# Performance work log

Hardware: AMD Instinct MI355X
Metric: run time of the kernel (lower is better)

## Reference

```python
import jax, jax.numpy as jnp
import numpy as np

B, SQ, SK, H, NH = 2, 2048, 2048, 2048, 16
HD = H // NH  # 128
NEG = -1e9


def setup_inputs() -> dict:
    key = jax.random.key(0)
    ks = jax.random.split(key, 8)
    hidden_states = jax.random.normal(ks[0], (B, SQ, H), dtype=jnp.float32)
    # key already transposed/expanded for baddbmm: [B*nh, head_dim, key_len]
    k = jax.random.normal(ks[1], (B * NH, HD, SK), dtype=jnp.float32)
    v = jax.random.normal(ks[2], (B, NH, SK, HD), dtype=jnp.float32)
    # additive float causal mask [B, 1, Sq, Sk]
    causal = jnp.tril(jnp.ones((SQ, SK), dtype=bool))
    attention_mask = jnp.where(causal, 0.0, NEG).astype(jnp.float32)
    attention_mask = jnp.broadcast_to(attention_mask[None, None], (B, 1, SQ, SK))
    w_q = jax.random.normal(ks[3], (H, H), dtype=jnp.float32) * 0.02
    b_q = jnp.zeros((H,), dtype=jnp.float32)
    w_proj = jax.random.normal(ks[4], (H, H), dtype=jnp.float32) * 0.02
    b_proj = jnp.zeros((H,), dtype=jnp.float32)
    return {
        "hidden_states": hidden_states,
        "key": k,
        "value": v,
        "attention_mask": attention_mask,
        "w_q": w_q,
        "b_q": b_q,
        "w_proj": w_proj,
        "b_proj": b_proj,
    }


def reference(hidden_states, key, value, attention_mask, w_q, b_q, w_proj, b_proj):
    dtype = hidden_states.dtype
    scale = 1.0 / (HD ** 0.5)  # scale_attn_weights=True, attention_multiplier=None
    # q projection: [B, Sq, H] -> [B, nh, Sq, hd]
    q = hidden_states @ w_q.T + b_q
    q = q.reshape(B, SQ, NH, HD).transpose(0, 2, 1, 3)
    # key comes in as [B*nh, hd, Sk]
    k = key.reshape(B, NH, HD, SK)
    # scores = mask + scale * q @ k  (baddbmm with beta=1)
    scores = attention_mask + scale * jnp.einsum("bhqd,bhdk->bhqk", q, k)
    # softmax in fp32 (attention_softmax_in_fp32=True), cast back
    probs = jax.nn.softmax(scores.astype(jnp.float32), axis=-1).astype(dtype)
    # attn_pdrop=0 -> no dropout
    out = jnp.einsum("bhqk,bhkd->bhqd", probs, value)  # [B, nh, Sq, hd]
    out = out.transpose(0, 2, 1, 3).reshape(B, SQ, H)
    out = out @ w_proj.T + b_proj  # resid_pdrop=0 -> no dropout
    return out
```

## Files before the change

### kernel.cpp

```cpp
#include <hip/hip_runtime.h>
#include <hip/hip_bf16.h>

typedef __bf16 bf16;
typedef __bf16 bf16x4 __attribute__((ext_vector_type(4)));
typedef __bf16 bf16x8 __attribute__((ext_vector_type(8)));
typedef float  f32x4  __attribute__((ext_vector_type(4)));
typedef float  f32x16 __attribute__((ext_vector_type(16)));
typedef unsigned int u32;

#define B_   2
#define SQ_  2048
#define SK_  2048
#define H_   2048
#define NH_  16
#define HD_  128
#define BH_  (B_*NH_)

__device__ inline void gl_lds16(const bf16* g, bf16* l) {
  __builtin_amdgcn_global_load_lds(
      (const __attribute__((address_space(1))) u32*)(const void*)g,
      (__attribute__((address_space(3))) u32*)(void*)l,
      16, 0, 0);
}

__device__ inline float exp2_fast(float x) {
  float r; asm("v_exp_f32 %0, %1" : "=v"(r) : "v"(x)); return r;
}

union PW { u32 w[4]; bf16x8 v; };

__global__ __launch_bounds__(256) void cvt3_f32_bf16(const float* __restrict__ a, bf16* __restrict__ ao,
                                                     const float* __restrict__ b, bf16* __restrict__ bo,
                                                     const float* __restrict__ c, bf16* __restrict__ co) {
  const int blk = blockIdx.x;
  const float* in; bf16* out; int n4, bstart, nblk;
  if (blk < 1024)      { in = a; out = ao; n4 = (B_ * SQ_ * H_) / 4; bstart = 0;    nblk = 1024; }
  else if (blk < 1536) { in = b; out = bo; n4 = (H_ * H_) / 4;       bstart = 1024; nblk = 512; }
  else                 { in = c; out = co; n4 = (H_ * H_) / 4;       bstart = 1536; nblk = 512; }
  int i = (blk - bstart) * 256 + threadIdx.x;
  const int stride = nblk * 256;
  for (; i < n4; i += stride) {
    float4 v = ((const float4*)in)[i];
    bf16x4 w; w[0] = (bf16)v.x; w[1] = (bf16)v.y; w[2] = (bf16)v.z; w[3] = (bf16)v.w;
    ((bf16x4*)out)[i] = w;
  }
}

__global__ __launch_bounds__(256) void transpose_cvt2(const float* __restrict__ key,
                                                      const float* __restrict__ value,
                                                      bf16* __restrict__ kout,
                                                      bf16* __restrict__ vout) {
  __shared__ float tile[64][65];
  const int id = blockIdx.x;
  const float* src; bf16* dst; int R, C, r0, c0, bh;
  if (id < 2048) {
    src = key; dst = kout; R = HD_; C = SK_;
    c0 = (id & 31) * 64; r0 = ((id >> 5) & 1) * 64; bh = id >> 6;
  } else {
    const int j = id - 2048;
    src = value; dst = vout; R = SK_; C = HD_;
    c0 = (j & 1) * 64; r0 = ((j >> 1) & 31) * 64; bh = j >> 6;
  }
  src += (size_t)bh * R * C;
  dst += (size_t)bh * R * C;
  const int t = threadIdx.x;
  const int tx = t & 15, ty = t >> 4;
#pragma unroll
  for (int p = 0; p < 4; ++p) {
    int rr = ty + p * 16;
    float4 v = *(const float4*)&src[(size_t)(r0 + rr) * C + c0 + tx * 4];
    tile[rr][tx * 4 + 0] = v.x; tile[rr][tx * 4 + 1] = v.y;
    tile[rr][tx * 4 + 2] = v.z; tile[rr][tx * 4 + 3] = v.w;
  }
  __syncthreads();
#pragma unroll
  for (int p = 0; p < 4; ++p) {
    int cc = ty + p * 16;
    bf16x4 w;
#pragma unroll
    for (int i = 0; i < 4; ++i) w[i] = (bf16)tile[tx * 4 + i][cc];
    *(bf16x4*)&dst[(size_t)(c0 + cc) * R + r0 + tx * 4] = w;
  }
}

template <typename OutT>
__global__ __launch_bounds__(256) void gemm_bt(const bf16* __restrict__ A,
                                               const bf16* __restrict__ Bw,
                                               const float* __restrict__ bias,
                                               OutT* __restrict__ C,
                                               int M, int N, int K, float osc) {
  __shared__ bf16 Abuf[128 * 32];
  __shared__ bf16 Bbuf[128 * 32];
  const int nbn = N >> 7;
  int wg = blockIdx.x, nwg = gridDim.x;
  int swz = (nwg & 7) ? wg : ((wg & 7) * (nwg >> 3) + (wg >> 3));
  int bm = swz / nbn, bn = swz % nbn;
  const int t = threadIdx.x, lane = t & 63, wid = t >> 6;
  const int r = lane & 15, g = lane >> 4;
  const int wr = wid >> 1, wc = wid & 1;
  const size_t m0 = (size_t)bm * 128, n0 = (size_t)bn * 128;

  f32x4 acc[4][4];
#pragma unroll
  for (int m = 0; m < 4; ++m)
#pragma unroll
    for (int n = 0; n < 4; ++n) acc[m][n] = (f32x4){0.f, 0.f, 0.f, 0.f};

  for (int k0 = 0; k0 < K; k0 += 32) {
    __syncthreads();
#pragma unroll
    for (int p = 0; p < 2; ++p) {
      int c = p * 256 + t;
      int row = c >> 2, off = c & 3;
      gl_lds16(A + (m0 + row) * K + k0 + off * 8, &Abuf[(p * 256 + wid * 64) * 8]);
      gl_lds16(Bw + (n0 + row) * K + k0 + off * 8, &Bbuf[(p * 256 + wid * 64) * 8]);
    }
    __syncthreads();
    bf16x8 af[4], bfr[4];
#pragma unroll
    for (int m = 0; m < 4; ++m)
      af[m] = *(const bf16x8*)&Abuf[(wr * 64 + m * 16 + r) * 32 + g * 8];
#pragma unroll
    for (int n = 0; n < 4; ++n)
      bfr[n] = *(const bf16x8*)&Bbuf[(wc * 64 + n * 16 + r) * 32 + g * 8];
#pragma unroll
    for (int m = 0; m < 4; ++m)
#pragma unroll
      for (int n = 0; n < 4; ++n)
        acc[m][n] = __builtin_amdgcn_mfma_f32_16x16x32_bf16(af[m], bfr[n], acc[m][n], 0, 0, 0);
  }

  float bv[4];
#pragma unroll
  for (int n = 0; n < 4; ++n) bv[n] = bias[n0 + wc * 64 + n * 16 + r];
#pragma unroll
  for (int m = 0; m < 4; ++m)
#pragma unroll
    for (int n = 0; n < 4; ++n)
#pragma unroll
      for (int rr = 0; rr < 4; ++rr) {
        size_t row = m0 + wr * 64 + m * 16 + g * 4 + rr;
        size_t col = n0 + wc * 64 + n * 16 + r;
        C[row * N + col] = (OutT)((acc[m][n][rr] + bv[n]) * osc);
      }
}

__global__ __launch_bounds__(256, 2) void flash_attn(const bf16* __restrict__ Q,
                                                     const bf16* __restrict__ Kt,
                                                     const bf16* __restrict__ Vt,
                                                     bf16* __restrict__ O,
                                                     bf16* __restrict__ part,
                                                     float2* __restrict__ mlbuf) {
  __shared__ bf16 Klds[2][64 * 128];
  __shared__ bf16 Vlds[2][128 * 64];

  const int id = blockIdx.x;
  const int pr = (id >> 3) & 7;
  const int hf = (id >> 6) & 1;
  const int bh = (id & 7) + 8 * (id >> 7);
  const int qtA = 15 - pr, qtB = pr;
  const int nA = 2 * qtA + 2, nB = 2 * qtB + 2;
  const int b = bh >> 4, h = bh & 15;
  const int t = threadIdx.x, lane = t & 63, wid = t >> 6;
  const int l5 = lane & 31, hiL = lane >> 5;

  const bf16* Kbase = Kt + (size_t)bh * SK_ * HD_;
  const bf16* Vbase = Vt + (size_t)bh * HD_ * SK_;

  u32 kSrc[4], vSrc[4];
#pragma unroll
  for (int p = 0; p < 4; ++p) {
    int c = p * 256 + t;
    { int row = c >> 4, off = c & 15, src = off ^ (row & 7);
      kSrc[p] = (u32)(row * HD_ + src * 8); }
    { int row = c >> 3, off = c & 7, src = off ^ (row & 7);
      vSrc[p] = (u32)(row * SK_ + src * 8); }
  }

  int cur = 0;
  const int npass = hf ? 2 : 1;
#pragma unroll 1
  for (int ps = 0; ps < npass; ++ps) {
    int qt, lo, hi, partial;
    if (!hf)          { qt = qtA; lo = 0;  hi = 17; partial = 1; }
    else if (ps == 0) { qt = qtA; lo = 17; hi = nA; partial = 1; }
    else              { qt = qtB; lo = 0;  hi = nB; partial = 0; }
    const int qbw = qt * 128 + wid * 32;
    const int q_lane = qbw + l5;

    bf16x8 qf[8];
    {
      const size_t qrow = (size_t)(b * SQ_ + q_lane) * H_ + (size_t)h * HD_;
#pragma unroll
      for (int dt = 0; dt < 8; ++dt)
        qf[dt] = *(const bf16x8*)&Q[qrow + dt * 16 + 8 * hiL];
    }

    f32x16 acc[4];
#pragma unroll
    for (int n = 0; n < 4; ++n)
#pragma unroll
      for (int e = 0; e < 16; ++e) acc[n][e] = 0.f;
    float mrun = -3.0e38f, lpart = 0.f;

    {
      const size_t ks = (size_t)lo * (64 * HD_), vs = (size_t)lo * 64;
#pragma unroll
      for (int p = 0; p < 4; ++p) {
        gl_lds16(Kbase + ks + kSrc[p], &Klds[cur][(p * 256 + wid * 64) * 8]);
        gl_lds16(Vbase + vs + vSrc[p], &Vlds[cur][(p * 256 + wid * 64) * 8]);
      }
    }
    asm volatile("s_waitcnt vmcnt(0)" ::: "memory");
    __syncthreads();

#pragma unroll 1
    for (int st = lo; st < hi; ++st) {
      if (st + 1 < hi) {
        const size_t ks = (size_t)(st + 1) * (64 * HD_), vs = (size_t)(st + 1) * 64;
#pragma unroll
        for (int p = 0; p < 4; ++p) {
          gl_lds16(Kbase + ks + kSrc[p], &Klds[cur ^ 1][(p * 256 + wid * 64) * 8]);
          gl_lds16(Vbase + vs + vSrc[p], &Vlds[cur ^ 1][(p * 256 + wid * 64) * 8]);
        }
      }
      const int s0 = st * 64;

      if (s0 <= qbw + 31) {
        f32x16 sv0, sv1;
#pragma unroll
        for (int e = 0; e < 16; ++e) { sv0[e] = 0.f; sv1[e] = 0.f; }
        __builtin_amdgcn_s_setprio(1);
#pragma unroll
        for (int dt = 0; dt < 8; ++dt) {
          const int dch = ((2 * dt + hiL) ^ (l5 & 7)) * 8;
          bf16x8 kf0 = *(const bf16x8*)&Klds[cur][l5 * 128 + dch];
          bf16x8 kf1 = *(const bf16x8*)&Klds[cur][(32 + l5) * 128 + dch];
          sv0 = __builtin_amdgcn_mfma_f32_32x32x16_bf16(kf0, qf[dt], sv0, 0, 0, 0);
          sv1 = __builtin_amdgcn_mfma_f32_32x32x16_bf16(kf1, qf[dt], sv1, 0, 0, 0);
        }
        __builtin_amdgcn_s_setprio(0);

        if (s0 + 63 > qbw) {
#pragma unroll
          for (int r2 = 0; r2 < 16; ++r2) {
            const int kl = (r2 & 3) + 8 * (r2 >> 2) + 4 * hiL;
            if (s0 + kl > q_lane)      sv0[r2] = -3.0e38f;
            if (s0 + 32 + kl > q_lane) sv1[r2] = -3.0e38f;
          }
        }

        float pm = -3.0e38f;
#pragma unroll
        for (int r2 = 0; r2 < 16; ++r2) pm = fmaxf(pm, fmaxf(sv0[r2], sv1[r2]));
        pm = fmaxf(pm, __shfl_xor(pm, 32));
        if (!__all(pm <= mrun + 10.0f ? 1 : 0)) {
          const float mnew = fmaxf(mrun, pm);
          const float corr = exp2_fast(mrun - mnew);
          mrun = mnew;
          lpart *= corr;
          const int cb = __float_as_int(corr);
#pragma unroll
          for (int r2 = 0; r2 < 16; ++r2) {
            const int q2 = (r2 & 3) + 8 * (r2 >> 2) + 4 * hiL;
            const float cc = __int_as_float(__builtin_amdgcn_ds_bpermute(q2 * 4, cb));
#pragma unroll
            for (int n = 0; n < 4; ++n) acc[n][r2] *= cc;
          }
        }

        float psum = 0.f;
#pragma unroll
        for (int r2 = 0; r2 < 16; ++r2) {
          sv0[r2] = exp2_fast(sv0[r2] - mrun); psum += sv0[r2];
          sv1[r2] = exp2_fast(sv1[r2] - mrun); psum += sv1[r2];
        }
        lpart += psum;

        bf16x8 pa[4];
#pragma unroll
        for (int h2 = 0; h2 < 2; ++h2) {
          u32 pk[8], px[8];
#pragma unroll
          for (int j = 0; j < 8; ++j) {
            union { bf16 hh[2]; u32 u; } tt;
            float plo = h2 ? sv1[2 * j] : sv0[2 * j];
            float phi = h2 ? sv1[2 * j + 1] : sv0[2 * j + 1];
            tt.hh[0] = (bf16)plo; tt.hh[1] = (bf16)phi;
            pk[j] = tt.u;
          }
#pragma unroll
          for (int j = 0; j < 8; ++j) px[j] = (u32)__shfl_xor((int)pk[j], 32);
          PW a0, a1;
          a0.w[0] = hiL ? px[2] : pk[0];
          a0.w[1] = hiL ? px[3] : pk[1];
          a0.w[2] = hiL ? pk[2] : px[0];
          a0.w[3] = hiL ? pk[3] : px[1];
          a1.w[0] = hiL ? px[6] : pk[4];
          a1.w[1] = hiL ? px[7] : pk[5];
          a1.w[2] = hiL ? pk[6] : px[4];
          a1.w[3] = hiL ? pk[7] : px[5];
          pa[2 * h2]     = a0.v;
          pa[2 * h2 + 1] = a1.v;
        }

        __builtin_amdgcn_s_setprio(1);
#pragma unroll
        for (int n = 0; n < 4; ++n) {
#pragma unroll
          for (int kt = 0; kt < 4; ++kt) {
            bf16x8 vf = *(const bf16x8*)&Vlds[cur][(n * 32 + l5) * 64 +
                                                   (((2 * kt + hiL) ^ (l5 & 7)) * 8)];
            acc[n] = __builtin_amdgcn_mfma_f32_32x32x16_bf16(pa[kt], vf, acc[n], 0, 0, 0);
          }
        }
        __builtin_amdgcn_s_setprio(0);
      }

      asm volatile("s_waitcnt vmcnt(0)" ::: "memory");
      __syncthreads();
      cur ^= 1;
    }

    float ltot = lpart + __shfl_xor(lpart, 32);
    if (partial) {
      const int slot = (hf * 8 + pr) * 32 + bh;
      bf16* pbase = part + (size_t)slot * (128 * 128);
#pragma unroll
      for (int n = 0; n < 4; ++n)
#pragma unroll
        for (int r2 = 0; r2 < 16; ++r2) {
          const int rowt = wid * 32 + (r2 & 3) + 8 * (r2 >> 2) + 4 * hiL;
          pbase[rowt * 128 + n * 32 + l5] = (bf16)acc[n][r2];
        }
      if (lane < 32)
        mlbuf[(size_t)slot * 128 + wid * 32 + lane] = float2{mrun, ltot};
    } else {
      const float inv = 1.0f / ltot;
      const int ib = __float_as_int(inv);
#pragma unroll
      for (int r2 = 0; r2 < 16; ++r2) {
        const int q2 = (r2 & 3) + 8 * (r2 >> 2) + 4 * hiL;
        const float ic = __int_as_float(__builtin_amdgcn_ds_bpermute(q2 * 4, ib));
        const size_t rowg = (size_t)(b * SQ_ + qbw + q2);
#pragma unroll
        for (int n = 0; n < 4; ++n)
          O[rowg * H_ + (size_t)h * HD_ + n * 32 + l5] = (bf16)(acc[n][r2] * ic);
      }
    }
  }
}

__global__ __launch_bounds__(256) void flash_merge(const bf16* __restrict__ part,
                                                   const float2* __restrict__ mlbuf,
                                                   bf16* __restrict__ O) {
  const int idx = blockIdx.x * 2 + (threadIdx.x >> 7);
  const int d = threadIdx.x & 127;
  const int row = idx & 127;
  const int bh = (idx >> 7) & 31;
  const int pr = idx >> 12;
  const int qtA = 15 - pr;
  const int b = bh >> 4, h = bh & 15;
  const int slot0 = pr * 32 + bh;
  const int slot1 = (8 + pr) * 32 + bh;
  const float2 ml0 = mlbuf[(size_t)slot0 * 128 + row];
  const float2 ml1 = mlbuf[(size_t)slot1 * 128 + row];
  const float M = fmaxf(ml0.x, ml1.x);
  const float c0 = exp2_fast(ml0.x - M);
  const float c1 = exp2_fast(ml1.x - M);
  const float inv = 1.0f / (c0 * ml0.y + c1 * ml1.y);
  const float a0 = (float)part[(size_t)slot0 * (128 * 128) + row * 128 + d];
  const float a1 = (float)part[(size_t)slot1 * (128 * 128) + row * 128 + d];
  const size_t orow = (size_t)(b * SQ_ + qtA * 128 + row);
  O[orow * H_ + (size_t)h * HD_ + d] = (bf16)((c0 * a0 + c1 * a1) * inv);
}

extern "C" void kernel_launch(void* const* d_in, const int* in_sizes, int n_in,
                              void* d_out, int out_size, void* d_ws, size_t ws_size,
                              hipStream_t stream) {
  const float* hidden = (const float*)d_in[0];
  const float* key    = (const float*)d_in[1];
  const float* value  = (const float*)d_in[2];
  const float* w_q    = (const float*)d_in[4];
  const float* b_q    = (const float*)d_in[5];
  const float* w_proj = (const float*)d_in[6];
  const float* b_proj = (const float*)d_in[7];
  float* out = (float*)d_out;

  const size_t N_HID = (size_t)B_ * SQ_ * H_;
  const size_t N_W   = (size_t)H_ * H_;
  const size_t N_KV  = (size_t)BH_ * SK_ * HD_;
  const float SC2 = 0.08838834764831845f * 1.4426950408889634f;

  bf16* hid_bf  = (bf16*)d_ws;
  bf16* wq_bf   = hid_bf + N_HID;
  bf16* wp_bf   = wq_bf + N_W;
  bf16* k_bf    = wp_bf + N_W;
  bf16* vt_bf   = k_bf + N_KV;
  bf16* q_bf    = vt_bf + N_KV;
  bf16* part_bf = q_bf + N_HID;
  float2* ml_bf = (float2*)(part_bf + (size_t)512 * 128 * 128);
  bf16* attn_bf = hid_bf;

  cvt3_f32_bf16<<<2048, 256, 0, stream>>>(hidden, hid_bf, w_q, wq_bf, w_proj, wp_bf);
  transpose_cvt2<<<4096, 256, 0, stream>>>(key, value, k_bf, vt_bf);

  gemm_bt<bf16><<<(B_ * SQ_ / 128) * (H_ / 128), 256, 0, stream>>>(
      hid_bf, wq_bf, b_q, q_bf, B_ * SQ_, H_, H_, SC2);

  flash_attn<<<512, 256, 0, stream>>>(q_bf, k_bf, vt_bf, attn_bf, part_bf, ml_bf);
  flash_merge<<<16384, 256, 0, stream>>>(part_bf, ml_bf, attn_bf);

  gemm_bt<float><<<(B_ * SQ_ / 128) * (H_ / 128), 256, 0, stream>>>(
      attn_bf, wp_bf, b_proj, out, B_ * SQ_, H_, H_, 1.0f);
}
```

Baseline: 215.6 us.

## Add flash attention variant with 256-row Q tiles, 32-key steps, and 4-way KV split

Adds a new flash attention kernel in which each wave handles 64 query rows (two 32-row MFMA tiles) and shares every K/V fragment read from LDS between both tiles. The key/value step drops to 32 columns. Causal work is balanced by pairing query tiles and splitting the KV range into four equal 18-step chunks, followed by a new merge kernel that combines up to four partial results. The aim is to halve LDS K/V traffic per MFMA and even out per-block load. In exchange it adds more partial-buffer writes, a larger merge launch, and a workspace-size check that falls back to the old path.

```diff
diff --git a/kernel.cpp b/kernel.cpp
--- a/kernel.cpp
+++ b/kernel.cpp
@@ -145,6 +145,278 @@
       }
 }
 
+__device__ __forceinline__ void sm32(f32x16& sv, float& mrun, float& lpart,
+                                     f32x16 (&acc)[4], bf16x8 (&pa)[2], int hiL) {
+  float pm = sv[0];
+#pragma unroll
+  for (int r2 = 1; r2 < 16; ++r2) pm = fmaxf(pm, sv[r2]);
+  pm = fmaxf(pm, __shfl_xor(pm, 32));
+  if (!__all(pm <= mrun + 10.0f ? 1 : 0)) {
+    const float mnew = fmaxf(mrun, pm);
+    const float corr = exp2_fast(mrun - mnew);
+    mrun = mnew; lpart *= corr;
+    const int cb = __float_as_int(corr);
+#pragma unroll
+    for (int r2 = 0; r2 < 16; ++r2) {
+      const int q2 = (r2 & 3) + 8 * (r2 >> 2) + 4 * hiL;
+      const float cc = __int_as_float(__builtin_amdgcn_ds_bpermute(q2 * 4, cb));
+#pragma unroll
+      for (int n = 0; n < 4; ++n) acc[n][r2] *= cc;
+    }
+  }
+  float psum = 0.f;
+#pragma unroll
+  for (int r2 = 0; r2 < 16; ++r2) { sv[r2] = exp2_fast(sv[r2] - mrun); psum += sv[r2]; }
+  lpart += psum;
+  u32 pk[8], px[8];
+#pragma unroll
+  for (int j = 0; j < 8; ++j) {
+    union { bf16 hh[2]; u32 u; } tt;
+    tt.hh[0] = (bf16)sv[2 * j]; tt.hh[1] = (bf16)sv[2 * j + 1];
+    pk[j] = tt.u;
+  }
+#pragma unroll
+  for (int j = 0; j < 8; ++j) px[j] = (u32)__shfl_xor((int)pk[j], 32);
+  PW a0, a1;
+  a0.w[0] = hiL ? px[2] : pk[0];  a0.w[1] = hiL ? px[3] : pk[1];
+  a0.w[2] = hiL ? pk[2] : px[0];  a0.w[3] = hiL ? pk[3] : px[1];
+  a1.w[0] = hiL ? px[6] : pk[4];  a1.w[1] = hiL ? px[7] : pk[5];
+  a1.w[2] = hiL ? pk[6] : px[4];  a1.w[3] = hiL ? pk[7] : px[5];
+  pa[0] = a0.v; pa[1] = a1.v;
+}
+
+__global__ __launch_bounds__(256, 2) void flash_attn2(const bf16* __restrict__ Q,
+                                                      const bf16* __restrict__ Kt,
+                                                      const bf16* __restrict__ Vt,
+                                                      bf16* __restrict__ O,
+                                                      bf16* __restrict__ part,
+                                                      float2* __restrict__ mlbuf) {
+  __shared__ bf16 Klds[2][32 * 128];
+  __shared__ bf16 Vlds[2][128 * 32];
+
+  const int id = blockIdx.x;
+  const int pr = (id >> 3) & 3;
+  const int qq = (id >> 5) & 3;
+  const int bh = (id & 7) + 8 * (id >> 7);
+  const int qtA = 7 - pr, qtB = pr;
+  const int nA = 8 * qtA + 8, nB = 8 * qtB + 8;
+  const int prefix = pr * 4 + (pr == 3 ? 1 : 0);
+  const int b = bh >> 4, h = bh & 15;
+  const int t = threadIdx.x, lane = t & 63, wid = t >> 6;
+  const int l5 = lane & 31, hiL = lane >> 5;
+
+  const bf16* Kbase = Kt + (size_t)bh * SK_ * HD_;
+  const bf16* Vbase = Vt + (size_t)bh * HD_ * SK_;
+
+  u32 kSrc[2], vSrc[2];
+#pragma unroll
+  for (int p2 = 0; p2 < 2; ++p2) {
+    int c = p2 * 256 + t;
+    { int row = c >> 4, off = c & 15, src = off ^ (row & 7);
+      kSrc[p2] = (u32)(row * HD_ + src * 8); }
+    { int row = c >> 2, off = c & 3, src = off ^ ((row >> 1) & 3);
+      vSrc[p2] = (u32)(row * SK_ + src * 8); }
+  }
+
+  const int lo_q = qq * 18, hi_q = lo_q + 18;
+  const bool hasA = (lo_q < nA);
+  const int aHi = hi_q < nA ? hi_q : nA;
+  const int bLo = (lo_q - nA > 0) ? (lo_q - nA) : 0;
+  const int bHi = hi_q - nA;
+  const bool hasB = (hi_q > nA);
+  const int npass = (hasA ? 1 : 0) + (hasB ? 1 : 0);
+
+  int cur = 0;
+#pragma unroll 1
+  for (int p = 0; p < npass; ++p) {
+    const bool isA = hasA && (p == 0);
+    const int qt = isA ? qtA : qtB;
+    const int lo = isA ? lo_q : bLo;
+    const int hi = isA ? aHi : bHi;
+    const bool direct = (!isA) && (bLo == 0) && (bHi == nB);
+    const int slotg = (prefix + (isA ? qq : qq + 1)) * 32 + bh;
+    const int qbw = qt * 256 + wid * 64;
+
+    bf16x8 qf0[8], qf1[8];
+    {
+      const size_t qr0 = (size_t)(b * SQ_ + qbw + l5) * H_ + (size_t)h * HD_;
+      const size_t qr1 = qr0 + (size_t)32 * H_;
+#pragma unroll
+      for (int dt = 0; dt < 8; ++dt) {
+        qf0[dt] = *(const bf16x8*)&Q[qr0 + dt * 16 + 8 * hiL];
+        qf1[dt] = *(const bf16x8*)&Q[qr1 + dt * 16 + 8 * hiL];
+      }
+    }
+
+    f32x16 acc0[4], acc1[4];
+#pragma unroll
+    for (int n = 0; n < 4; ++n)
+#pragma unroll
+      for (int e = 0; e < 16; ++e) { acc0[n][e] = 0.f; acc1[n][e] = 0.f; }
+    float mrun0 = -3.0e38f, lpart0 = 0.f, mrun1 = -3.0e38f, lpart1 = 0.f;
+
+    {
+      const size_t ks = (size_t)lo * (32 * HD_), vs = (size_t)lo * 32;
+#pragma unroll
+      for (int p2 = 0; p2 < 2; ++p2) {
+        gl_lds16(Kbase + ks + kSrc[p2], &Klds[cur][(p2 * 256 + wid * 64) * 8]);
+        gl_lds16(Vbase + vs + vSrc[p2], &Vlds[cur][(p2 * 256 + wid * 64) * 8]);
+      }
+    }
+    asm volatile("s_waitcnt vmcnt(0)" ::: "memory");
+    __syncthreads();
+
+#pragma unroll 1
+    for (int st = lo; st < hi; ++st) {
+      if (st + 1 < hi) {
+        const size_t ks = (size_t)(st + 1) * (32 * HD_), vs = (size_t)(st + 1) * 32;
+#pragma unroll
+        for (int p2 = 0; p2 < 2; ++p2) {
+          gl_lds16(Kbase + ks + kSrc[p2], &Klds[cur ^ 1][(p2 * 256 + wid * 64) * 8]);
+          gl_lds16(Vbase + vs + vSrc[p2], &Vlds[cur ^ 1][(p2 * 256 + wid * 64) * 8]);
+        }
+      }
+      const int s0 = st * 32;
+      if (s0 <= qbw + 63) {
+        const bool g0a = (s0 <= qbw + 31);
+        f32x16 sv0, sv1;
+#pragma unroll
+        for (int e = 0; e < 16; ++e) { sv0[e] = 0.f; sv1[e] = 0.f; }
+        __builtin_amdgcn_s_setprio(1);
+        if (g0a) {
+#pragma unroll
+          for (int dt = 0; dt < 8; ++dt) {
+            bf16x8 kf = *(const bf16x8*)&Klds[cur][l5 * 128 + (((2 * dt + hiL) ^ (l5 & 7)) * 8)];
+            sv0 = __builtin_amdgcn_mfma_f32_32x32x16_bf16(kf, qf0[dt], sv0, 0, 0, 0);
+            sv1 = __builtin_amdgcn_mfma_f32_32x32x16_bf16(kf, qf1[dt], sv1, 0, 0, 0);
+          }
+        } else {
+#pragma unroll
+          for (int dt = 0; dt < 8; ++dt) {
+            bf16x8 kf = *(const bf16x8*)&Klds[cur][l5 * 128 + (((2 * dt + hiL) ^ (l5 & 7)) * 8)];
+            sv1 = __builtin_amdgcn_mfma_f32_32x32x16_bf16(kf, qf1[dt], sv1, 0, 0, 0);
+          }
+        }
+        __builtin_amdgcn_s_setprio(0);
+
+        if (g0a && s0 + 31 > qbw) {
+#pragma unroll
+          for (int r2 = 0; r2 < 16; ++r2) {
+            const int kl = (r2 & 3) + 8 * (r2 >> 2) + 4 * hiL;
+            if (s0 + kl > qbw + l5) sv0[r2] = -3.0e38f;
+          }
+        }
+        if (s0 + 31 > qbw + 32) {
+#pragma unroll
+          for (int r2 = 0; r2 < 16; ++r2) {
+            const int kl = (r2 & 3) + 8 * (r2 >> 2) + 4 * hiL;
+            if (s0 + kl > qbw + 32 + l5) sv1[r2] = -3.0e38f;
+          }
+        }
+
+        bf16x8 pa0[2], pa1[2];
+        if (g0a) sm32(sv0, mrun0, lpart0, acc0, pa0, hiL);
+        sm32(sv1, mrun1, lpart1, acc1, pa1, hiL);
+
+        __builtin_amdgcn_s_setprio(1);
+        if (g0a) {
+#pragma unroll
+          for (int n = 0; n < 4; ++n)
+#pragma unroll
+            for (int kt = 0; kt < 2; ++kt) {
+              bf16x8 vf = *(const bf16x8*)&Vlds[cur][(n * 32 + l5) * 32 +
+                                                     (((2 * kt + hiL) ^ ((l5 >> 1) & 3)) * 8)];
+              acc0[n] = __builtin_amdgcn_mfma_f32_32x32x16_bf16(pa0[kt], vf, acc0[n], 0, 0, 0);
+              acc1[n] = __builtin_amdgcn_mfma_f32_32x32x16_bf16(pa1[kt], vf, acc1[n], 0, 0, 0);
+            }
+        } else {
+#pragma unroll
+          for (int n = 0; n < 4; ++n)
+#pragma unroll
+            for (int kt = 0; kt < 2; ++kt) {
+              bf16x8 vf = *(const bf16x8*)&Vlds[cur][(n * 32 + l5) * 32 +
+                                                     (((2 * kt + hiL) ^ ((l5 >> 1) & 3)) * 8)];
+              acc1[n] = __builtin_amdgcn_mfma_f32_32x32x16_bf16(pa1[kt], vf, acc1[n], 0, 0, 0);
+            }
+        }
+        __builtin_amdgcn_s_setprio(0);
+      }
+      asm volatile("s_waitcnt vmcnt(0)" ::: "memory");
+      __syncthreads();
+      cur ^= 1;
+    }
+
+    const float lt0 = lpart0 + __shfl_xor(lpart0, 32);
+    const float lt1 = lpart1 + __shfl_xor(lpart1, 32);
+    if (direct) {
+      const int ib0 = __float_as_int(1.0f / lt0);
+      const int ib1 = __float_as_int(1.0f / lt1);
+#pragma unroll
+      for (int r2 = 0; r2 < 16; ++r2) {
+        const int q2 = (r2 & 3) + 8 * (r2 >> 2) + 4 * hiL;
+        const float ic0 = __int_as_float(__builtin_amdgcn_ds_bpermute(q2 * 4, ib0));
+        const float ic1 = __int_as_float(__builtin_amdgcn_ds_bpermute(q2 * 4, ib1));
+        const size_t r0g = (size_t)(b * SQ_ + qbw + q2);
+#pragma unroll
+        for (int n = 0; n < 4; ++n) {
+          O[r0g * H_ + (size_t)h * HD_ + n * 32 + l5] = (bf16)(acc0[n][r2] * ic0);
+          O[(r0g + 32) * H_ + (size_t)h * HD_ + n * 32 + l5] = (bf16)(acc1[n][r2] * ic1);
+        }
+      }
+    } else {
+      bf16* pbase = part + (size_t)slotg * (256 * 128);
+#pragma unroll
+      for (int r2 = 0; r2 < 16; ++r2) {
+        const int q2 = (r2 & 3) + 8 * (r2 >> 2) + 4 * hiL;
+        const int rl = wid * 64 + q2;
+#pragma unroll
+        for (int n = 0; n < 4; ++n) {
+          pbase[rl * 128 + n * 32 + l5] = (bf16)acc0[n][r2];
+          pbase[(rl + 32) * 128 + n * 32 + l5] = (bf16)acc1[n][r2];
+        }
+      }
+      if (lane < 32) {
+        mlbuf[(size_t)slotg * 256 + wid * 64 + lane] = float2{mrun0, lt0};
+        mlbuf[(size_t)slotg * 256 + wid * 64 + 32 + lane] = float2{mrun1, lt1};
+      }
+    }
+  }
+}
+
+__global__ __launch_bounds__(256) void flash_merge2(const bf16* __restrict__ part,
+                                                    const float2* __restrict__ mlbuf,
+                                                    bf16* __restrict__ O) {
+  const int ridx = blockIdx.x * 2 + (threadIdx.x >> 7);
+  const int d = threadIdx.x & 127;
+  const int row = ridx & 255;
+  const int bh = (ridx >> 8) & 31;
+  const int u = ridx >> 13;
+  const int pr = (u < 4) ? u : (u - 2);
+  const int qt = (u < 4) ? (7 - pr) : pr;
+  const int nseg = (u < 4) ? ((pr < 2) ? 4 : 3) : 2;
+  const int prefix = pr * 4 + (pr == 3 ? 1 : 0);
+  const int slot0 = prefix + ((u < 4) ? 0 : 3);
+  const int b = bh >> 4, h = bh & 15;
+  float ms[4], ls[4];
+  float M = -3.0e38f;
+#pragma unroll
+  for (int s = 0; s < 4; ++s)
+    if (s < nseg) {
+      float2 ml = mlbuf[(size_t)((slot0 + s) * 32 + bh) * 256 + row];
+      ms[s] = ml.x; ls[s] = ml.y;
+      M = fmaxf(M, ml.x);
+    }
+  float denom = 0.f, val = 0.f;
+#pragma unroll
+  for (int s = 0; s < 4; ++s)
+    if (s < nseg) {
+      const float c = exp2_fast(ms[s] - M);
+      denom += c * ls[s];
+      val += c * (float)part[(size_t)((slot0 + s) * 32 + bh) * (256 * 128) + row * 128 + d];
+    }
+  O[(size_t)(b * SQ_ + qt * 256 + row) * H_ + (size_t)h * HD_ + d] = (bf16)(val / denom);
+}
+
 __global__ __launch_bounds__(256, 2) void flash_attn(const bf16* __restrict__ Q,
                                                      const bf16* __restrict__ Kt,
                                                      const bf16* __restrict__ Vt,
@@ -153,7 +425,6 @@
                                                      float2* __restrict__ mlbuf) {
   __shared__ bf16 Klds[2][64 * 128];
   __shared__ bf16 Vlds[2][128 * 64];
-
   const int id = blockIdx.x;
   const int pr = (id >> 3) & 7;
   const int hf = (id >> 6) & 1;
@@ -163,10 +434,8 @@
   const int b = bh >> 4, h = bh & 15;
   const int t = threadIdx.x, lane = t & 63, wid = t >> 6;
   const int l5 = lane & 31, hiL = lane >> 5;
-
   const bf16* Kbase = Kt + (size_t)bh * SK_ * HD_;
   const bf16* Vbase = Vt + (size_t)bh * HD_ * SK_;
-
   u32 kSrc[4], vSrc[4];
 #pragma unroll
   for (int p = 0; p < 4; ++p) {
@@ -176,7 +445,6 @@
     { int row = c >> 3, off = c & 7, src = off ^ (row & 7);
       vSrc[p] = (u32)(row * SK_ + src * 8); }
   }
-
   int cur = 0;
   const int npass = hf ? 2 : 1;
 #pragma unroll 1
@@ -187,22 +455,18 @@
     else              { qt = qtB; lo = 0;  hi = nB; partial = 0; }
     const int qbw = qt * 128 + wid * 32;
     const int q_lane = qbw + l5;
-
     bf16x8 qf[8];
     {
       const size_t qrow = (size_t)(b * SQ_ + q_lane) * H_ + (size_t)h * HD_;
 #pragma unroll
-      for (int dt = 0; dt < 8; ++dt)
-        qf[dt] = *(const bf16x8*)&Q[qrow + dt * 16 + 8 * hiL];
-    }
-
+      for (int dt = 0; dt < 8; ++dt) qf[dt] = *(const bf16x8*)&Q[qrow + dt * 16 + 8 * hiL];
+    }
     f32x16 acc[4];
 #pragma unroll
     for (int n = 0; n < 4; ++n)
 #pragma unroll
       for (int e = 0; e < 16; ++e) acc[n][e] = 0.f;
     float mrun = -3.0e38f, lpart = 0.f;
-
     {
       const size_t ks = (size_t)lo * (64 * HD_), vs = (size_t)lo * 64;
 #pragma unroll
@@ -213,7 +477,6 @@
     }
     asm volatile("s_waitcnt vmcnt(0)" ::: "memory");
     __syncthreads();
-
 #pragma unroll 1
     for (int st = lo; st < hi; ++st) {
       if (st + 1 < hi) {
@@ -225,7 +488,6 @@
         }
       }
       const int s0 = st * 64;
-
       if (s0 <= qbw + 31) {
         f32x16 sv0, sv1;
 #pragma unroll
@@ -240,7 +502,6 @@
           sv1 = __builtin_amdgcn_mfma_f32_32x32x16_bf16(kf1, qf[dt], sv1, 0, 0, 0);
         }
         __builtin_amdgcn_s_setprio(0);
-
         if (s0 + 63 > qbw) {
 #pragma unroll
           for (int r2 = 0; r2 < 16; ++r2) {
@@ -249,7 +510,6 @@
             if (s0 + 32 + kl > q_lane) sv1[r2] = -3.0e38f;
           }
         }
-
         float pm = -3.0e38f;
 #pragma unroll
         for (int r2 = 0; r2 < 16; ++r2) pm = fmaxf(pm, fmaxf(sv0[r2], sv1[r2]));
@@ -257,8 +517,7 @@
         if (!__all(pm <= mrun + 10.0f ? 1 : 0)) {
           const float mnew = fmaxf(mrun, pm);
           const float corr = exp2_fast(mrun - mnew);
-          mrun = mnew;
-          lpart *= corr;
+          mrun = mnew; lpart *= corr;
           const int cb = __float_as_int(corr);
 #pragma unroll
           for (int r2 = 0; r2 < 16; ++r2) {
@@ -268,7 +527,6 @@
             for (int n = 0; n < 4; ++n) acc[n][r2] *= cc;
           }
         }
-
         float psum = 0.f;
 #pragma unroll
         for (int r2 = 0; r2 < 16; ++r2) {
@@ -276,7 +534,6 @@
           sv1[r2] = exp2_fast(sv1[r2] - mrun); psum += sv1[r2];
         }
         lpart += psum;
-
         bf16x8 pa[4];
 #pragma unroll
         for (int h2 = 0; h2 < 2; ++h2) {
@@ -292,18 +549,12 @@
 #pragma unroll
           for (int j = 0; j < 8; ++j) px[j] = (u32)__shfl_xor((int)pk[j], 32);
           PW a0, a1;
-          a0.w[0] = hiL ? px[2] : pk[0];
-          a0.w[1] = hiL ? px[3] : pk[1];
-          a0.w[2] = hiL ? pk[2] : px[0];
-          a0.w[3] = hiL ? pk[3] : px[1];
-          a1.w[0] = hiL ? px[6] : pk[4];
-          a1.w[1] = hiL ? px[7] : pk[5];
-          a1.w[2] = hiL ? pk[6] : px[4];
-          a1.w[3] = hiL ? pk[7] : px[5];
-          pa[2 * h2]     = a0.v;
-          pa[2 * h2 + 1] = a1.v;
-        }
-
+          a0.w[0] = hiL ? px[2] : pk[0]; a0.w[1] = hiL ? px[3] : pk[1];
+          a0.w[2] = hiL ? pk[2] : px[0]; a0.w[3] = hiL ? pk[3] : px[1];
+          a1.w[0] = hiL ? px[6] : pk[4]; a1.w[1] = hiL ? px[7] : pk[5];
+          a1.w[2] = hiL ? pk[6] : px[4]; a1.w[3] = hiL ? pk[7] : px[5];
+          pa[2 * h2] = a0.v; pa[2 * h2 + 1] = a1.v;
+        }
         __builtin_amdgcn_s_setprio(1);
 #pragma unroll
         for (int n = 0; n < 4; ++n) {
@@ -316,12 +567,10 @@
         }
         __builtin_amdgcn_s_setprio(0);
       }
-
       asm volatile("s_waitcnt vmcnt(0)" ::: "memory");
       __syncthreads();
       cur ^= 1;
     }
-
     float ltot = lpart + __shfl_xor(lpart, 32);
     if (partial) {
       const int slot = (hf * 8 + pr) * 32 + bh;
@@ -399,8 +648,11 @@
   bf16* vt_bf   = k_bf + N_KV;
   bf16* q_bf    = vt_bf + N_KV;
   bf16* part_bf = q_bf + N_HID;
-  float2* ml_bf = (float2*)(part_bf + (size_t)512 * 128 * 128);
   bf16* attn_bf = hid_bf;
+
+  const size_t PART2_EL = (size_t)576 * 256 * 128;
+  float2* ml2 = (float2*)(part_bf + PART2_EL);
+  const size_t need2 = (size_t)((char*)(ml2 + (size_t)576 * 256) - (char*)d_ws);
 
   cvt3_f32_bf16<<<2048, 256, 0, stream>>>(hidden, hid_bf, w_q, wq_bf, w_proj, wp_bf);
   transpose_cvt2<<<4096, 256, 0, stream>>>(key, value, k_bf, vt_bf);
@@ -408,8 +660,14 @@
   gemm_bt<bf16><<<(B_ * SQ_ / 128) * (H_ / 128), 256, 0, stream>>>(
       hid_bf, wq_bf, b_q, q_bf, B_ * SQ_, H_, H_, SC2);
 
-  flash_attn<<<512, 256, 0, stream>>>(q_bf, k_bf, vt_bf, attn_bf, part_bf, ml_bf);
-  flash_merge<<<16384, 256, 0, stream>>>(part_bf, ml_bf, attn_bf);
+  if (ws_size >= need2) {
+    flash_attn2<<<512, 256, 0, stream>>>(q_bf, k_bf, vt_bf, attn_bf, part_bf, ml2);
+    flash_merge2<<<24576, 256, 0, stream>>>(part_bf, ml2, attn_bf);
+  } else {
+    float2* ml1 = (float2*)(part_bf + (size_t)512 * 128 * 128);
+    flash_attn<<<512, 256, 0, stream>>>(q_bf, k_bf, vt_bf, attn_bf, part_bf, ml1);
+    flash_merge<<<16384, 256, 0, stream>>>(part_bf, ml1, attn_bf);
+  }
 
   gemm_bt<float><<<(B_ * SQ_ / 128) * (H_ / 128), 256, 0, stream>>>(
       attn_bf, wp_bf, b_proj, out, B_ * SQ_, H_, H_, 1.0f);
```

Measured after the change: 338.4 us. +57.0%, slower.
